# Kernel tuning notes

Measured on AMD Instinct MI355X. Metric: run time of the kernel, lower is better.

Reference implementation:

```python
import jax, jax.numpy as jnp
import numpy as np

K = 3        # deform conv kernel size
STRIDE = 1
PAD = 1
DIL = 1


def setup_inputs() -> dict:
    key = jax.random.key(0)
    k1, k2, k3, k4 = jax.random.split(key, 4)
    B, C, H, W, O = 4, 256, 96, 96, 256
    x = jax.random.normal(k1, (B, C, H, W), jnp.float32)
    # offset-predicting conv: 3x3, stride 1, pad 1 -> 2*K*K channels
    # (source inits these to zero; use small random weights so offsets are
    # nonzero but sub-pixel scale, exercising the bilinear-sampling path)
    w_off = jax.random.normal(k2, (2 * K * K, C, 3, 3), jnp.float32) * 0.01
    b_off = jnp.zeros((2 * K * K,), jnp.float32)
    w_dc = jax.random.normal(k3, (O, C, K, K), jnp.float32) * (1.0 / np.sqrt(C * K * K))
    b_dc = jax.random.normal(k4, (O,), jnp.float32) * 0.01
    return {"x": x, "w_off": w_off, "b_off": b_off, "w_dc": w_dc, "b_dc": b_dc}


def _conv2d(x, w, b, stride, pad):
    out = jax.lax.conv_general_dilated(
        x, w, window_strides=(stride, stride),
        padding=[(pad, pad), (pad, pad)],
        dimension_numbers=("NCHW", "OIHW", "NCHW"))
    return out + b[None, :, None, None]


def _deform_conv(x, offset, w_dc, b_dc):
    # x: [B,C,H,W]; offset: [B, 2*K*K, Ho, Wo]; w_dc: [O,C,K,K]
    B, C, H, W = x.shape
    O = w_dc.shape[0]
    Ho = (H + 2 * PAD - DIL * (K - 1) - 1) // STRIDE + 1
    Wo = (W + 2 * PAD - DIL * (K - 1) - 1) // STRIDE + 1
    # mmcv layout: channel = (i*K + j)*2 + {0: dy, 1: dx}
    off = offset.reshape(B, K * K, 2, Ho, Wo)
    iy = jnp.repeat(jnp.arange(K), K)   # kernel row index per tap  [K*K]
    jx = jnp.tile(jnp.arange(K), K)     # kernel col index per tap  [K*K]
    base_y = (jnp.arange(Ho) * STRIDE - PAD)[None, :, None] + (iy * DIL)[:, None, None]  # [K2,Ho,1]
    base_x = (jnp.arange(Wo) * STRIDE - PAD)[None, None, :] + (jx * DIL)[:, None, None]  # [K2,1,Wo]
    py = base_y[None].astype(x.dtype) + off[:, :, 0]  # [B,K2,Ho,Wo]
    px = base_x[None].astype(x.dtype) + off[:, :, 1]  # [B,K2,Ho,Wo]

    y0 = jnp.floor(py)
    x0 = jnp.floor(px)
    ly = py - y0
    lx = px - x0
    y0i = y0.astype(jnp.int32)
    x0i = x0.astype(jnp.int32)

    flat = x.reshape(B, C, H * W)

    def corner(yi, xi, wgt):
        # zero-padding bilinear: out-of-range corners contribute 0
        valid = ((yi >= 0) & (yi < H) & (xi >= 0) & (xi < W)).astype(x.dtype)
        idx = jnp.clip(yi, 0, H - 1) * W + jnp.clip(xi, 0, W - 1)  # [B,K2,Ho,Wo]
        g = jnp.take_along_axis(flat, idx.reshape(B, 1, -1), axis=2)
        g = g.reshape(B, C, K * K, Ho, Wo)
        return g * (wgt * valid)[:, None]  # broadcast over channels

    val = (corner(y0i, x0i, (1 - ly) * (1 - lx))
           + corner(y0i, x0i + 1, (1 - ly) * lx)
           + corner(y0i + 1, x0i, ly * (1 - lx))
           + corner(y0i + 1, x0i + 1, ly * lx))  # [B,C,K2,Ho,Wo]

    out = jnp.einsum("bckhw,ock->bohw", val, w_dc.reshape(O, C, K * K))
    return out + b_dc[None, :, None, None]


def reference(x, w_off, b_off, w_dc, b_dc):
    offset = _conv2d(x, w_off, b_off, stride=1, pad=1)  # [B, 2*K*K, H, W]
    return _deform_conv(x, offset, w_dc, b_dc)
```

## Files before the change

### kernel.cpp

```cpp
#include <hip/hip_runtime.h>
#include <hip/hip_fp16.h>
#include <math.h>

#define BB   4
#define CC   256
#define HH   96
#define WW   96
#define OO   256
#define HW   9216
#define KDIM 2304
#define OFFC 18
#define NKC  36


typedef short bf16x8 __attribute__((ext_vector_type(8)));
typedef float f32x4  __attribute__((ext_vector_type(4)));
typedef unsigned int u32x4 __attribute__((ext_vector_type(4)));

#define WS_V_SZ    (36864ull * 4608ull)
#define WS_WB_OFF  WS_V_SZ
#define WS_WB_SZ   (256ull * 4608ull)
#define WS_META_OFF (WS_WB_OFF + WS_WB_SZ)
#define WS_META_SZ (4ull * 9ull * 9216ull * 16ull)
#define WS_WOFF_OFF (WS_META_OFF + 0x200000ull)
#define WS_NEED    (WS_META_OFF + WS_META_SZ)

__device__ __forceinline__ unsigned short f2bfu(float f) {
    unsigned u = __float_as_uint(f);
    unsigned r = (u + 0x7fffu + ((u >> 16) & 1u)) >> 16;
    return (unsigned short)r;
}
__device__ __forceinline__ unsigned pack2(float lo, float hi) {
    return (unsigned)f2bfu(lo) | ((unsigned)f2bfu(hi) << 16);
}
__device__ __forceinline__ void gload16(const void* g, void* l) {
    __builtin_amdgcn_global_load_lds((const __attribute__((address_space(1))) void*)g,
                                     (__attribute__((address_space(3))) void*)l, 16, 0, 0);
}

__device__ __forceinline__ uint4 make_meta(int pr, int t, float dy, float dx) {
    int oh = pr / WW, ow = pr - oh * WW;
    float py = (float)(oh - 1 + t / 3) + dy;
    float px = (float)(ow - 1 + (t % 3)) + dx;
    float y0f = floorf(py), x0f = floorf(px);
    int y0 = (int)y0f, x0 = (int)x0f;
    float ly = py - y0f, lx = px - x0f;
    float wy0 = (y0 >= 0 && y0 < HH) ? 1.f - ly : 0.f;
    float wy1 = (y0 + 1 >= 0 && y0 + 1 < HH) ? ly : 0.f;
    float u0 = (x0 >= 0 && x0 < WW) ? 1.f - lx : 0.f;
    float u1 = (x0 + 1 >= 0 && x0 + 1 < WW) ? lx : 0.f;
    int pb = min(max(x0, 0), WW - 2);
    float s0, s1;
    if (x0 < 0)           { s0 = u1; s1 = 0.f; }
    else if (x0 > WW - 2) { s0 = 0.f; s1 = u0; }
    else                  { s0 = u0; s1 = u1; }
    int cy0 = min(max(y0, 0), HH - 1);
    int cy1 = min(max(y0 + 1, 0), HH - 1);
    uint4 m;
    m.x = (unsigned)(cy0 * WW + pb);
    m.y = (unsigned)(cy1 * WW + pb);
    m.z = pack2(wy0 * s0, wy0 * s1);
    m.w = pack2(wy1 * s0, wy1 * s1);
    return m;
}


__global__ __launch_bounds__(256)
void woff_kernel(const float* __restrict__ w_off, char* __restrict__ Woff_b)
{
    int kc  = blockIdx.x;
    int tid = threadIdx.x;
    int so  = tid >> 3, sq = tid & 7;
    int tap = kc >> 2, cb = (kc & 3) * 64;
    uint4 pk; pk.x = pk.y = pk.z = pk.w = 0u;
    if (so < OFFC) {
        const float* wr = w_off + (size_t)so * KDIM + (size_t)(cb + sq * 8) * 9 + tap;
        float wv[8];
        #pragma unroll
        for (int i = 0; i < 8; ++i) wv[i] = wr[i * 9];
        pk.x = pack2(wv[0], wv[1]); pk.y = pack2(wv[2], wv[3]);
        pk.z = pack2(wv[4], wv[5]); pk.w = pack2(wv[6], wv[7]);
    }
    *(uint4*)(Woff_b + (size_t)kc * 4096 + so * 128 + ((sq * 16) ^ ((so & 7) << 4))) = pk;
}

__global__ __launch_bounds__(512)
void offset_meta_kernel2(const float* __restrict__ x,
                         const char* __restrict__ Woff_b,
                         const float* __restrict__ b_off,
                         unsigned* __restrict__ meta2_ws)
{
    __shared__ __align__(16) char Asw[64 * 128];
    __shared__ __align__(16) char Wl[32 * 128];
    __shared__ float Dsh[64][21];

    const int tid = threadIdx.x;
    const int fin = ((blockIdx.x & 7) * 72) + (blockIdx.x >> 3);
    const int b   = fin / 144;
    const int pr0 = (fin % 144) * 64;
    const float* xb = x + (size_t)b * CC * HW;

    const int w    = tid >> 6;
    const int l15  = tid & 15;
    const int l4   = (tid >> 4) & 3;
    const int pf   = w & 3;
    const int of   = w >> 2;
    const int sp   = tid & 63;
    const int kq   = tid >> 6;

    const int prg = pr0 + sp;
    const int oh = prg / WW, ow = prg - (prg / WW) * WW;

    f32x4 acc = (f32x4){0.f, 0.f, 0.f, 0.f};

    for (int kc = 0; kc < NKC; ++kc) {
        const int tap = kc >> 2;
        const int cb  = (kc & 3) * 64;
        if (w < 4)
            gload16(Woff_b + (size_t)kc * 4096 + (size_t)tid * 16, Wl + w * 1024);
        {
            int iy = oh + tap / 3 - 1;
            int ix = ow + tap % 3 - 1;
            bool ok = (iy >= 0) & (iy < HH) & (ix >= 0) & (ix < WW);
            const float* xp = xb + (size_t)(cb + kq * 8) * HW + iy * WW + ix;
            float v[8];
            #pragma unroll
            for (int e = 0; e < 8; ++e)
                v[e] = ok ? xp[(size_t)e * HW] : 0.f;
            uint4 pk;
            pk.x = pack2(v[0], v[1]); pk.y = pack2(v[2], v[3]);
            pk.z = pack2(v[4], v[5]); pk.w = pack2(v[6], v[7]);
            *(uint4*)(Asw + sp * 128 + ((kq * 16) ^ ((sp & 7) << 4))) = pk;
        }
        __syncthreads();
        {
            int p_loc = pf * 16 + l15;
            unsigned aswz = (unsigned)((p_loc & 7) << 4);
            int o_loc = of * 16 + l15;
            unsigned oswz = (unsigned)((o_loc & 7) << 4);
            #pragma unroll
            for (int ks = 0; ks < 2; ++ks) {
                bf16x8 a  = *(const bf16x8*)(Asw + p_loc * 128 + ((ks * 64 + l4 * 16) ^ aswz));
                bf16x8 bw = *(const bf16x8*)(Wl + o_loc * 128 + ((ks * 64 + l4 * 16) ^ oswz));
                acc = __builtin_amdgcn_mfma_f32_16x16x32_bf16(a, bw, acc, 0, 0, 0);
            }
        }
        __syncthreads();
    }

    {
        int o = of * 16 + l15;
        if (o < OFFC) {
            float bo = b_off[o];
            #pragma unroll
            for (int r = 0; r < 4; ++r)
                Dsh[pf * 16 + l4 * 4 + r][o] = acc[r] + bo;
        }
    }
    __syncthreads();
    for (int s = tid; s < 9 * 64; s += 512) {
        int t = s >> 6, pl = s & 63;
        int pr = pr0 + pl;
        float dy = Dsh[pl][2 * t];
        float dx = Dsh[pl][2 * t + 1];
        unsigned lo = (unsigned)__half_as_ushort(__float2half(dy));
        unsigned hi = (unsigned)__half_as_ushort(__float2half(dx));
        meta2_ws[((size_t)b * 9 + t) * HW + pr] = lo | (hi << 16);
    }
}

__global__ __launch_bounds__(256)
void wconv_kernel(const float* __restrict__ w_dc, char* __restrict__ wb)
{
    int idx = blockIdx.x * 256 + (int)threadIdx.x;
    int o   = idx / 288;
    int rem = idx - o * 288;
    int ch  = rem >> 3;
    int q   = rem & 7;
    int tap = ch >> 2;
    int c0  = (ch & 3) * 64 + q * 8;
    const float* wr = w_dc + (size_t)o * KDIM + (size_t)c0 * 9 + tap;
    float wv[8];
    #pragma unroll
    for (int i = 0; i < 8; ++i) wv[i] = wr[i * 9];
    uint4 pk;
    pk.x = pack2(wv[0], wv[1]); pk.y = pack2(wv[2], wv[3]);
    pk.z = pack2(wv[4], wv[5]); pk.w = pack2(wv[6], wv[7]);
    *(uint4*)(wb + (size_t)o * 4608 + ch * 128 + ((q * 16) ^ ((o & 7) << 4))) = pk;
}

#define GT_P   576
#define GT_WIN 14
__global__ __launch_bounds__(512, 4)
void gather_kernel9(const float* __restrict__ x,
                    const unsigned* __restrict__ meta2,
                    char* __restrict__ Vg)
{
    __shared__ __align__(16) unsigned short Xs[GT_WIN * 2 * 100 * 8];
    __shared__ unsigned Md[9 * GT_P];

    int bid  = blockIdx.x;
    int fin  = (bid & 7) * 128 + (bid >> 3);
    int tile = fin >> 4;
    int cq   = fin & 15;
    int b    = tile >> 4;
    int h0   = (tile & 15) * 6;
    int c0   = cq * 16;
    int tid  = threadIdx.x;
    int prow0 = tile * GT_P;

    int r0 = h0 - 3; r0 = r0 < 0 ? 0 : (r0 > 82 ? 82 : r0);

    for (int s = tid; s < 9 * GT_P; s += 512) {
        int t = s / GT_P, pl = s - t * GT_P;
        Md[s] = meta2[((size_t)b * 9 + t) * HW + h0 * WW + pl];
    }

    const float* xb = x + ((size_t)b * CC + c0) * HW + r0 * WW;
    for (int s = tid; s < GT_WIN * 2 * 96; s += 512) {
        int col = s % 96;
        int rem = s / 96;
        int chh = rem & 1;
        int row = rem >> 1;
        const float* g = xb + (size_t)(chh * 8) * HW + row * WW + col;
        uint4 pk;
        pk.x = pack2(g[0],              g[(size_t)1 * HW]);
        pk.y = pack2(g[(size_t)2 * HW], g[(size_t)3 * HW]);
        pk.z = pack2(g[(size_t)4 * HW], g[(size_t)5 * HW]);
        pk.w = pack2(g[(size_t)6 * HW], g[(size_t)7 * HW]);
        *(uint4*)&Xs[(((row * 2 + chh) * 100) + col) * 8] = pk;
    }
    __syncthreads();

    const int chh  = tid & 1;
    const int lsub = (tid & 63) >> 1;
    const int w    = tid >> 6;
    const float* xg = x + ((size_t)b * CC + c0 + chh * 8) * HW;
    const int chunk_hi = (cq >> 2) * 128;
    const int base_in_chunk = (cq & 3) * 32 + chh * 16;

    for (int pass = 0; pass < 3; ++pass) {
        int i = pass * 256 + w * 32 + lsub;
        if (i >= GT_P) break;
        int oh = h0 + i / WW, ow = i - (i / WW) * WW;
        char* vrow0 = Vg + (size_t)(prow0 + i) * 4608;
        const int inchunk = base_in_chunk ^ ((i & 7) << 4);
        #pragma unroll
        for (int t = 0; t < 9; ++t) {
            unsigned md = Md[t * GT_P + i];
            float dy = __half2float(__ushort_as_half((unsigned short)(md & 0xffffu)));
            float dx = __half2float(__ushort_as_half((unsigned short)(md >> 16)));
            float py = (float)(oh - 1 + t / 3) + dy;
            float px = (float)(ow - 1 + t % 3) + dx;
            float y0f = floorf(py), x0f = floorf(px);
            int y0 = (int)y0f, x0 = (int)x0f;
            float ly = py - y0f, lx = px - x0f;
            float wy0 = (y0 >= 0 && y0 < HH) ? 1.f - ly : 0.f;
            float wy1 = (y0 + 1 >= 0 && y0 + 1 < HH) ? ly : 0.f;
            float u0 = (x0 >= 0 && x0 < WW) ? 1.f - lx : 0.f;
            float u1 = (x0 + 1 >= 0 && x0 + 1 < WW) ? lx : 0.f;
            int pb = min(max(x0, 0), WW - 2);
            float s0, s1;
            if (x0 < 0)           { s0 = u1; s1 = 0.f; }
            else if (x0 > WW - 2) { s0 = 0.f; s1 = u0; }
            else                  { s0 = u0; s1 = u1; }
            int cy0 = min(max(y0, 0), HH - 1);
            int cy1 = min(max(y0 + 1, 0), HH - 1);
            float wa0 = wy0 * s0, wa1 = wy0 * s1;
            float wb0 = wy1 * s0, wb1 = wy1 * s1;
            float v[8];
            if (cy0 >= r0 && cy1 <= r0 + GT_WIN - 1) {
                int ra = ((cy0 - r0) * 2 + chh) * 100;
                int rb = ((cy1 - r0) * 2 + chh) * 100;
                u32x4 a0 = *(const u32x4*)&Xs[(ra + pb) * 8];
                u32x4 a1 = *(const u32x4*)&Xs[(ra + pb + 1) * 8];
                u32x4 b0 = *(const u32x4*)&Xs[(rb + pb) * 8];
                u32x4 b1 = *(const u32x4*)&Xs[(rb + pb + 1) * 8];
                #pragma unroll
                for (int k = 0; k < 8; ++k) {
                    unsigned sa0 = a0[k >> 1], sa1 = a1[k >> 1];
                    unsigned sb0 = b0[k >> 1], sb1 = b1[k >> 1];
                    float A0 = __uint_as_float((k & 1) ? (sa0 & 0xffff0000u) : (sa0 << 16));
                    float A1 = __uint_as_float((k & 1) ? (sa1 & 0xffff0000u) : (sa1 << 16));
                    float B0 = __uint_as_float((k & 1) ? (sb0 & 0xffff0000u) : (sb0 << 16));
                    float B1 = __uint_as_float((k & 1) ? (sb1 & 0xffff0000u) : (sb1 << 16));
                    v[k] = fmaf(wa0, A0, fmaf(wa1, A1, fmaf(wb0, B0, wb1 * B1)));
                }
            } else {
                const float* pa = xg + cy0 * WW + pb;
                const float* pq = xg + cy1 * WW + pb;
                #pragma unroll
                for (int k = 0; k < 8; ++k) {
                    float A0 = pa[(size_t)k * HW], A1 = pa[(size_t)k * HW + 1];
                    float B0 = pq[(size_t)k * HW], B1 = pq[(size_t)k * HW + 1];
                    v[k] = fmaf(wa0, A0, fmaf(wa1, A1, fmaf(wb0, B0, wb1 * B1)));
                }
            }
            u32x4 pk;
            pk.x = pack2(v[0], v[1]); pk.y = pack2(v[2], v[3]);
            pk.z = pack2(v[4], v[5]); pk.w = pack2(v[6], v[7]);
            *(u32x4*)(vrow0 + t * 512 + chunk_hi + inchunk) = pk;
        }
    }
}

__global__ __launch_bounds__(512)
void gemm_kernel(const char* __restrict__ Vg, const char* __restrict__ Wb,
                 const float* __restrict__ b_dc, float* __restrict__ out)
{
    __shared__ __align__(16) char Ab[2][128 * 128];
    __shared__ __align__(16) char Bb[2][128 * 128];

    int bid = blockIdx.x;
    int swzb = (bid & 7) * 72 + (bid >> 3);
    int pt = swzb >> 1, ot = swzb & 1;
    int tid = threadIdx.x;
    int wav = tid >> 6;
    const int l15 = tid & 15, l4 = (tid >> 4) & 3;
    const int wp = wav >> 2, wo = wav & 3;

    const char* Ag = Vg + (size_t)(pt * 128) * 4608;
    const char* Bg = Wb + (size_t)(ot * 128) * 4608;

    f32x4 acc[4][2];
    #pragma unroll
    for (int f = 0; f < 4; ++f)
        #pragma unroll
        for (int g = 0; g < 2; ++g)
            acc[f][g] = (f32x4){0.f, 0.f, 0.f, 0.f};

#define STAGE(bufi, t) {                                                         \
        const char* ag = Ag + (size_t)(t) * 128;                                 \
        const char* bg = Bg + (size_t)(t) * 128;                                 \
        _Pragma("unroll")                                                        \
        for (int i = 0; i < 2; ++i) {                                            \
            int u = i * 512 + tid;                                               \
            int row = u >> 3, cu = (u & 7) * 16;                                 \
            gload16(ag + (size_t)row * 4608 + cu,                                \
                    &Ab[bufi][(i * 512 + wav * 64) * 16]);                       \
            gload16(bg + (size_t)row * 4608 + cu,                                \
                    &Bb[bufi][(i * 512 + wav * 64) * 16]);                       \
        } }

    STAGE(0, 0);
    STAGE(1, 1);

    for (int t = 0; t < NKC; ++t) {
        int cb = t & 1;
        if (t < NKC - 1) {
            asm volatile("s_waitcnt vmcnt(4)" ::: "memory");
        } else {
            asm volatile("s_waitcnt vmcnt(0)" ::: "memory");
        }
        __builtin_amdgcn_s_barrier();
        asm volatile("" ::: "memory");
        #pragma unroll
        for (int ks = 0; ks < 2; ++ks) {
            bf16x8 a[4], bw[2];
            #pragma unroll
            for (int f = 0; f < 4; ++f) {
                int p_loc = wp * 64 + f * 16 + l15;
                a[f] = *(const bf16x8*)(Ab[cb] + p_loc * 128 +
                                        ((ks * 64 + l4 * 16) ^ ((p_loc & 7) << 4)));
            }
            #pragma unroll
            for (int g = 0; g < 2; ++g) {
                int o_loc = wo * 32 + g * 16 + l15;
                bw[g] = *(const bf16x8*)(Bb[cb] + o_loc * 128 +
                                         ((ks * 64 + l4 * 16) ^ ((o_loc & 7) << 4)));
            }
            #pragma unroll
            for (int f = 0; f < 4; ++f)
                #pragma unroll
                for (int g = 0; g < 2; ++g)
                    acc[f][g] = __builtin_amdgcn_mfma_f32_16x16x32_bf16(a[f], bw[g], acc[f][g], 0, 0, 0);
        }
        asm volatile("s_waitcnt lgkmcnt(0)" ::: "memory");
        __builtin_amdgcn_s_barrier();
        asm volatile("" ::: "memory");
        if (t + 2 < NKC) STAGE(cb, t + 2);
    }
#undef STAGE

    int b = pt / 72;
    int posr = (pt - b * 72) * 128;
    #pragma unroll
    for (int g = 0; g < 2; ++g) {
        int og = ot * 128 + wo * 32 + g * 16 + l15;
        float bias = b_dc[og];
        float* op = out + ((size_t)b * OO + og) * HW + posr + wp * 64 + l4 * 4;
        #pragma unroll
        for (int f = 0; f < 4; ++f) {
            f32x4 r = acc[f][g];
            float4 st;
            st.x = r[0] + bias; st.y = r[1] + bias;
            st.z = r[2] + bias; st.w = r[3] + bias;
            *(float4*)(op + f * 16) = st;
        }
    }
}


__global__ __launch_bounds__(256)
void offset_conv6_kernel(const float* __restrict__ x,
                         const float* __restrict__ w_off,
                         const float* __restrict__ b_off,
                         float* __restrict__ off)
{
    int bid   = blockIdx.x;
    int g     = bid % 3;
    int chunk = (bid / 3) % 36;
    int b     = bid / 108;
    int ocb   = g * 6;
    int pr    = chunk * 256 + (int)threadIdx.x;
    int oh    = pr / WW, ow = pr % WW;
    const float* xb = x + (size_t)b * CC * HW;

    float acc[6];
    #pragma unroll
    for (int i = 0; i < 6; ++i) acc[i] = b_off[ocb + i];

    bool interior = (oh >= 1) & (oh < HH - 1) & (ow >= 1) & (ow < WW - 1);
    if (interior) {
        const float* xp = xb + (oh - 1) * WW + (ow - 1);
        float xv[9];
        #pragma unroll
        for (int t = 0; t < 9; ++t) xv[t] = xp[(t / 3) * WW + (t % 3)];
        for (int c = 0; c < CC; ++c) {
            float xn[9];
            if (c + 1 < CC) {
                const float* xq = xp + (size_t)(c + 1) * HW;
                #pragma unroll
                for (int t = 0; t < 9; ++t) xn[t] = xq[(t / 3) * WW + (t % 3)];
            }
            #pragma unroll
            for (int i = 0; i < 6; ++i) {
                const float* wr = w_off + ((size_t)(ocb + i) * CC + c) * 9;
                #pragma unroll
                for (int t = 0; t < 9; ++t)
                    acc[i] = fmaf(xv[t], wr[t], acc[i]);
            }
            #pragma unroll
            for (int t = 0; t < 9; ++t) xv[t] = xn[t];
        }
    } else {
        for (int c = 0; c < CC; ++c) {
            const float* xc = xb + (size_t)c * HW;
            float xv[9];
            #pragma unroll
            for (int t = 0; t < 9; ++t) {
                int yy = oh + t / 3 - 1, xx = ow + t % 3 - 1;
                xv[t] = (yy >= 0 && yy < HH && xx >= 0 && xx < WW) ? xc[yy * WW + xx] : 0.f;
            }
            #pragma unroll
            for (int i = 0; i < 6; ++i) {
                const float* wr = w_off + ((size_t)(ocb + i) * CC + c) * 9;
                #pragma unroll
                for (int t = 0; t < 9; ++t)
                    acc[i] = fmaf(xv[t], wr[t], acc[i]);
            }
        }
    }
    #pragma unroll
    for (int i = 0; i < 6; ++i)
        off[((size_t)b * OFFC + ocb + i) * HW + pr] = acc[i];
}

__global__ __launch_bounds__(256)
void deform_mfma_kernel(const float* __restrict__ x,
                        const float* __restrict__ off,
                        const float* __restrict__ w_dc,
                        const float* __restrict__ b_dc,
                        float* __restrict__ out)
{
    __shared__ __align__(16) char VlB[128 * 128];
    __shared__ __align__(16) char WlB[128 * 128];
    __shared__ uint4 meta[9][128];

    const int tid  = threadIdx.x;
    const int ot   = blockIdx.x / 288;
    const int pt   = blockIdx.x % 288;
    const int pos0 = pt * 128;
    const int b    = pos0 / HW;
    const int posr = pos0 - b * HW;

    const float* offp = off + (size_t)b * OFFC * HW;
    for (int s = tid; s < 9 * 128; s += 256) {
        int tt = s >> 7, j = s & 127;
        int pr = posr + j;
        float dy = offp[(2 * tt) * HW + pr];
        float dx = offp[(2 * tt + 1) * HW + pr];
        meta[tt][j] = make_meta(pr, tt, dy, dx);
    }
    __syncthreads();

    const int l15 = tid & 15;
    const int l4  = (tid >> 4) & 3;
    const int wav = tid >> 6;
    const int wp  = wav >> 1, wwo = wav & 1;
    const int j     = tid & 127;
    const int khalf = tid >> 7;
    const int wo_o  = tid >> 4;
    const int wk    = (tid & 15) * 4;

    const float* wbase = w_dc + (size_t)(ot * 128) * KDIM;

    f32x4 acc[4][4];
    #pragma unroll
    for (int f = 0; f < 4; ++f)
        #pragma unroll
        for (int g = 0; g < 4; ++g)
            acc[f][g] = (f32x4){0.f, 0.f, 0.f, 0.f};

    for (int k0 = 0; k0 < KDIM; k0 += 64) {
        #pragma unroll
        for (int r = 0; r < 8; ++r) {
            int o = r * 16 + wo_o;
            const float4 wv = *(const float4*)(wbase + (size_t)o * KDIM + k0 + wk);
            uint2 u;
            u.x = pack2(wv.x, wv.y);
            u.y = pack2(wv.z, wv.w);
            *(uint2*)(WlB + o * 128 + ((wk * 2) ^ ((o & 7) << 4))) = u;
        }
        {
            unsigned kb = (unsigned)(k0 + khalf * 32);
            unsigned c  = kb / 9u;
            unsigned tt = kb - c * 9u;
            const float* xc = x + (size_t)((unsigned)b * CC + c) * HW;
            char* vrow = VlB + j * 128;
            const unsigned swz = (unsigned)((j & 7) << 4);
            #pragma unroll
            for (int g = 0; g < 4; ++g) {
                float v[8];
                #pragma unroll
                for (int e = 0; e < 8; ++e) {
                    uint4 m = meta[tt][j];
                    float A0 = xc[m.x], A1 = xc[m.x + 1];
                    float B0 = xc[m.y], B1 = xc[m.y + 1];
                    float a0 = __uint_as_float(m.z << 16);
                    float a1 = __uint_as_float(m.z & 0xffff0000u);
                    float b0 = __uint_as_float(m.w << 16);
                    float b1 = __uint_as_float(m.w & 0xffff0000u);
                    v[e] = fmaf(a0, A0, fmaf(a1, A1, fmaf(b0, B0, b1 * B1)));
                    ++tt;
                    if (tt == 9u) { tt = 0u; xc += HW; }
                }
                uint4 pk;
                pk.x = pack2(v[0], v[1]); pk.y = pack2(v[2], v[3]);
                pk.z = pack2(v[4], v[5]); pk.w = pack2(v[6], v[7]);
                *(uint4*)(vrow + (((unsigned)(khalf * 64 + g * 16)) ^ swz)) = pk;
            }
        }
        __syncthreads();

        #pragma unroll
        for (int ks = 0; ks < 2; ++ks) {
            bf16x8 a[4], bw[4];
            #pragma unroll
            for (int f = 0; f < 4; ++f) {
                int p_loc = wp * 64 + f * 16 + l15;
                a[f] = *(const bf16x8*)(VlB + p_loc * 128 +
                                        ((ks * 64 + l4 * 16) ^ ((p_loc & 7) << 4)));
            }
            #pragma unroll
            for (int g = 0; g < 4; ++g) {
                int o_loc = wwo * 64 + g * 16 + l15;
                bw[g] = *(const bf16x8*)(WlB + o_loc * 128 +
                                         ((ks * 64 + l4 * 16) ^ ((o_loc & 7) << 4)));
            }
            #pragma unroll
            for (int f = 0; f < 4; ++f)
                #pragma unroll
                for (int g = 0; g < 4; ++g)
                    acc[f][g] = __builtin_amdgcn_mfma_f32_16x16x32_bf16(a[f], bw[g], acc[f][g], 0, 0, 0);
        }
        __syncthreads();
    }

    #pragma unroll
    for (int g = 0; g < 4; ++g) {
        int og = ot * 128 + wwo * 64 + g * 16 + l15;
        float bias = b_dc[og];
        float* op = out + ((size_t)b * OO + og) * HW + posr + wp * 64 + l4 * 4;
        #pragma unroll
        for (int f = 0; f < 4; ++f) {
            f32x4 r = acc[f][g];
            float4 st;
            st.x = r[0] + bias; st.y = r[1] + bias;
            st.z = r[2] + bias; st.w = r[3] + bias;
            *(float4*)(op + f * 16) = st;
        }
    }
}

extern "C" void kernel_launch(void* const* d_in, const int* in_sizes, int n_in,
                              void* d_out, int out_size, void* d_ws, size_t ws_size,
                              hipStream_t stream)
{
    const float* x     = (const float*)d_in[0];
    const float* w_off = (const float*)d_in[1];
    const float* b_off = (const float*)d_in[2];
    const float* w_dc  = (const float*)d_in[3];
    const float* b_dc  = (const float*)d_in[4];
    float* out = (float*)d_out;

    if (ws_size >= WS_NEED) {
        char*     ws    = (char*)d_ws;
        char*     Vg    = ws;
        char*     Wb    = ws + WS_WB_OFF;
        unsigned* meta2 = (unsigned*)(ws + WS_META_OFF);
        char*     Woffb = ws + WS_WOFF_OFF;
        woff_kernel<<<NKC, 256, 0, stream>>>(w_off, Woffb);
        wconv_kernel<<<288, 256, 0, stream>>>(w_dc, Wb);
        offset_meta_kernel2<<<576, 512, 0, stream>>>(x, Woffb, b_off, meta2);
        gather_kernel9<<<1024, 512, 0, stream>>>(x, meta2, Vg);
        gemm_kernel<<<576, 512, 0, stream>>>(Vg, Wb, b_dc, out);
    } else {
        float* off = (float*)d_ws;
        offset_conv6_kernel<<<BB * 36 * 3, 256, 0, stream>>>(x, w_off, b_off, off);
        deform_mfma_kernel<<<(OO / 128) * (BB * HW / 128), 256, 0, stream>>>(x, off, w_dc, b_dc, out);
    }
}
```

Baseline: 179.4 us.

## Widen GEMM tile to full 256 output channels with triple-buffered loads

The deform-conv GEMM now gives each block a 128-position by 256-output tile instead of 128x128, which halves the grid to 288 blocks and doubles the accumulators per wave. Each A tile is loaded once rather than twice. The shared-memory pipeline also goes from double to triple buffering, with waitcnt values adjusted so loads are issued three stages ahead. In exchange, LDS use rises to about 144KB, register pressure goes up, and 288 blocks may fill the 256 CUs unevenly.

Result: slower. 202.4 us (+12.8%).

```diff
diff --git a/kernel.cpp b/kernel.cpp
--- a/kernel.cpp
+++ b/kernel.cpp
@@ -305,58 +305,60 @@
 }
 
 __global__ __launch_bounds__(512)
-void gemm_kernel(const char* __restrict__ Vg, const char* __restrict__ Wb,
-                 const float* __restrict__ b_dc, float* __restrict__ out)
-{
-    __shared__ __align__(16) char Ab[2][128 * 128];
-    __shared__ __align__(16) char Bb[2][128 * 128];
+void gemm_kernel2(const char* __restrict__ Vg, const char* __restrict__ Wb,
+                  const float* __restrict__ b_dc, float* __restrict__ out)
+{
+    __shared__ __align__(16) char Ab[3][128 * 128];
+    __shared__ __align__(16) char Bb[3][256 * 128];
 
     int bid = blockIdx.x;
-    int swzb = (bid & 7) * 72 + (bid >> 3);
-    int pt = swzb >> 1, ot = swzb & 1;
+    int pt  = (bid & 7) * 36 + (bid >> 3);
     int tid = threadIdx.x;
     int wav = tid >> 6;
     const int l15 = tid & 15, l4 = (tid >> 4) & 3;
     const int wp = wav >> 2, wo = wav & 3;
 
-    const char* Ag = Vg + (size_t)(pt * 128) * 4608;
-    const char* Bg = Wb + (size_t)(ot * 128) * 4608;
-
-    f32x4 acc[4][2];
+    const char* Ag = Vg + (size_t)pt * 128 * 4608;
+    const char* Bg = Wb;
+
+    f32x4 acc[4][4];
     #pragma unroll
     for (int f = 0; f < 4; ++f)
         #pragma unroll
-        for (int g = 0; g < 2; ++g)
+        for (int g = 0; g < 4; ++g)
             acc[f][g] = (f32x4){0.f, 0.f, 0.f, 0.f};
 
-#define STAGE(bufi, t) {                                                         \
+#define STG(bufi, t) {                                                           \
         const char* ag = Ag + (size_t)(t) * 128;                                 \
         const char* bg = Bg + (size_t)(t) * 128;                                 \
         _Pragma("unroll")                                                        \
         for (int i = 0; i < 2; ++i) {                                            \
             int u = i * 512 + tid;                                               \
-            int row = u >> 3, cu = (u & 7) * 16;                                 \
-            gload16(ag + (size_t)row * 4608 + cu,                                \
+            gload16(ag + (size_t)(u >> 3) * 4608 + (u & 7) * 16,                 \
                     &Ab[bufi][(i * 512 + wav * 64) * 16]);                       \
-            gload16(bg + (size_t)row * 4608 + cu,                                \
+        }                                                                        \
+        _Pragma("unroll")                                                        \
+        for (int i = 0; i < 4; ++i) {                                            \
+            int u = i * 512 + tid;                                               \
+            gload16(bg + (size_t)(u >> 3) * 4608 + (u & 7) * 16,                 \
                     &Bb[bufi][(i * 512 + wav * 64) * 16]);                       \
         } }
 
-    STAGE(0, 0);
-    STAGE(1, 1);
+    STG(0, 0);
+    STG(1, 1);
+    STG(2, 2);
 
     for (int t = 0; t < NKC; ++t) {
-        int cb = t & 1;
-        if (t < NKC - 1) {
-            asm volatile("s_waitcnt vmcnt(4)" ::: "memory");
-        } else {
-            asm volatile("s_waitcnt vmcnt(0)" ::: "memory");
-        }
+        int cb = t % 3;
+        int rem = NKC - t;
+        if (rem >= 3)      { asm volatile("s_waitcnt vmcnt(12)" ::: "memory"); }
+        else if (rem == 2) { asm volatile("s_waitcnt vmcnt(6)"  ::: "memory"); }
+        else               { asm volatile("s_waitcnt vmcnt(0)"  ::: "memory"); }
         __builtin_amdgcn_s_barrier();
         asm volatile("" ::: "memory");
         #pragma unroll
         for (int ks = 0; ks < 2; ++ks) {
-            bf16x8 a[4], bw[2];
+            bf16x8 a[4], bw[4];
             #pragma unroll
             for (int f = 0; f < 4; ++f) {
                 int p_loc = wp * 64 + f * 16 + l15;
@@ -364,29 +366,29 @@
                                         ((ks * 64 + l4 * 16) ^ ((p_loc & 7) << 4)));
             }
             #pragma unroll
-            for (int g = 0; g < 2; ++g) {
-                int o_loc = wo * 32 + g * 16 + l15;
+            for (int g = 0; g < 4; ++g) {
+                int o_loc = wo * 64 + g * 16 + l15;
                 bw[g] = *(const bf16x8*)(Bb[cb] + o_loc * 128 +
                                          ((ks * 64 + l4 * 16) ^ ((o_loc & 7) << 4)));
             }
             #pragma unroll
             for (int f = 0; f < 4; ++f)
                 #pragma unroll
-                for (int g = 0; g < 2; ++g)
+                for (int g = 0; g < 4; ++g)
                     acc[f][g] = __builtin_amdgcn_mfma_f32_16x16x32_bf16(a[f], bw[g], acc[f][g], 0, 0, 0);
         }
         asm volatile("s_waitcnt lgkmcnt(0)" ::: "memory");
         __builtin_amdgcn_s_barrier();
         asm volatile("" ::: "memory");
-        if (t + 2 < NKC) STAGE(cb, t + 2);
-    }
-#undef STAGE
+        if (t + 3 < NKC) STG(cb, t + 3);
+    }
+#undef STG
 
     int b = pt / 72;
     int posr = (pt - b * 72) * 128;
     #pragma unroll
-    for (int g = 0; g < 2; ++g) {
-        int og = ot * 128 + wo * 32 + g * 16 + l15;
+    for (int g = 0; g < 4; ++g) {
+        int og = wo * 64 + g * 16 + l15;
         float bias = b_dc[og];
         float* op = out + ((size_t)b * OO + og) * HW + posr + wp * 64 + l4 * 4;
         #pragma unroll
@@ -614,7 +616,7 @@
         wconv_kernel<<<288, 256, 0, stream>>>(w_dc, Wb);
         offset_meta_kernel2<<<576, 512, 0, stream>>>(x, Woffb, b_off, meta2);
         gather_kernel9<<<1024, 512, 0, stream>>>(x, meta2, Vg);
-        gemm_kernel<<<576, 512, 0, stream>>>(Vg, Wb, b_dc, out);
+        gemm_kernel2<<<288, 512, 0, stream>>>(Vg, Wb, b_dc, out);
     } else {
         float* off = (float*)d_ws;
         offset_conv6_kernel<<<BB * 36 * 3, 256, 0, stream>>>(x, w_off, b_off, off);
```
